# Kernel optimization log

Hardware: AMD Instinct MI355X
Metric: run time of the kernel (lower is better)

The kernel has to match this reference:

```python
import jax, jax.numpy as jnp
import numpy as np

HEADS = 4
DIM_HEAD = 32
SCALE = DIM_HEAD ** -0.5
EPS = 1e-5


def setup_inputs() -> dict:
    key = jax.random.key(0)
    ks = jax.random.split(key, 4)
    x = jax.random.normal(ks[0], (8, 64, 32, 32, 32), dtype=jnp.float32)
    w_qkv = jax.random.normal(ks[1], (384, 64), dtype=jnp.float32) * 0.05
    w_out = jax.random.normal(ks[2], (64, 128), dtype=jnp.float32) * 0.05
    b_out = jax.random.normal(ks[3], (64,), dtype=jnp.float32) * 0.05
    gamma = jnp.ones((64,), dtype=jnp.float32)
    beta = jnp.zeros((64,), dtype=jnp.float32)
    return {"x": x, "w_qkv": w_qkv, "w_out": w_out, "b_out": b_out,
            "gamma": gamma, "beta": beta}


def reference(x, w_qkv, w_out, b_out, gamma, beta):
    b, c, l, h, w = x.shape
    n = l * h * w
    xf = x.reshape(b, c, n)
    # 1x1 Conv3d (no bias) == channel matmul
    qkv = jnp.einsum('oc,bcn->bon', w_qkv, xf)            # [b, 3*H*D, n]
    q, k, v = jnp.split(qkv, 3, axis=1)
    def to_heads(t):
        return t.reshape(b, HEADS, DIM_HEAD, n)            # [b, H, D, n]
    q, k, v = to_heads(q), to_heads(k), to_heads(v)
    q = jax.nn.softmax(q, axis=2) * SCALE                  # softmax over head dim
    k = jax.nn.softmax(k, axis=3)                          # softmax over tokens
    context = jnp.einsum('bhdn,bhen->bhde', k, v)          # [b, H, D, D]
    out = jnp.einsum('bhde,bhdn->bhen', context, q)        # [b, H, D, n]
    out = out.reshape(b, HEADS * DIM_HEAD, n)
    # to_out: 1x1 Conv3d with bias, then GroupNorm(1, dim)
    out = jnp.einsum('oc,bcn->bon', w_out, out) + b_out[None, :, None]
    mu = out.mean(axis=(1, 2), keepdims=True)
    var = out.var(axis=(1, 2), keepdims=True)
    out = (out - mu) * jax.lax.rsqrt(var + EPS)
    out = out * gamma[None, :, None] + beta[None, :, None]
    return out.reshape(b, c, l, h, w)
```

## Files before the change

### kernel.cpp

```cpp
#include <hip/hip_runtime.h>

typedef unsigned short u16;
typedef __bf16 bf16;
typedef __bf16 bf16x8 __attribute__((ext_vector_type(8)));
typedef float f32x4 __attribute__((ext_vector_type(4)));

#define NTOK 32768
#define SCALE_F 0.17677669529663689f

__device__ __forceinline__ u16 f2bf(float f){
  unsigned u = __builtin_bit_cast(unsigned, f);
  u += 0x7fffu + ((u>>16)&1u);
  return (u16)(u>>16);
}
__device__ __forceinline__ float bf2f(u16 u){
  unsigned v = ((unsigned)u)<<16;
  return __builtin_bit_cast(float, v);
}

__global__ __launch_bounds__(256) void k1_ctx(const float* __restrict__ x,
    const float* __restrict__ wqkv, float* __restrict__ ctxP, float* __restrict__ s1P)
{
  const int b = blockIdx.y, chunk = blockIdx.x;
  const int t = threadIdx.x, w = t>>6, l = t&63, lr = l&15, lg = l>>4;
  __shared__ u16 xT[64*72];
  __shared__ u16 ek[128*72];
  __shared__ u16 vl[128*72];

  bf16x8 afr[4][2];
  #pragma unroll
  for (int rt=0;rt<4;rt++)
    #pragma unroll
    for (int ks=0;ks<2;ks++){
      const float* src = wqkv + (128 + w*64 + rt*16 + lr)*64 + ks*32 + lg*8;
      #pragma unroll
      for (int j=0;j<8;j++) ((u16*)&afr[rt][ks])[j] = f2bf(src[j]);
    }

  f32x4 ctx[2][2];
  #pragma unroll
  for (int i=0;i<2;i++)
    #pragma unroll
    for (int j=0;j<2;j++) ctx[i][j] = f32x4{0.f,0.f,0.f,0.f};
  float s1a = 0.f;
  const float* xb = x + (long)b*64*NTOK;

  for (int s=0; s<8; s++) {
    const int n0 = chunk*512 + s*64;
    __syncthreads();
    {
      const int c = t>>2, j0 = (t&3)*16;
      #pragma unroll
      for (int i=0;i<4;i++){
        f32x4 v4 = *(const f32x4*)(xb + (long)c*NTOK + n0 + j0 + i*4);
        #pragma unroll
        for (int j=0;j<4;j++) xT[(j0+i*4+j)*72 + c] = f2bf(v4[j]);
      }
    }
    __syncthreads();
    f32x4 acc[4][4];
    #pragma unroll
    for (int rt=0;rt<4;rt++)
      #pragma unroll
      for (int ct=0;ct<4;ct++) acc[rt][ct] = f32x4{0.f,0.f,0.f,0.f};
    #pragma unroll
    for (int ks=0;ks<2;ks++){
      bf16x8 bfr[4];
      #pragma unroll
      for (int ct=0;ct<4;ct++)
        bfr[ct] = *(const bf16x8*)&xT[(ct*16+lr)*72 + ks*32 + lg*8];
      #pragma unroll
      for (int rt=0;rt<4;rt++){
        #pragma unroll
        for (int ct=0;ct<4;ct++)
          acc[rt][ct] = __builtin_amdgcn_mfma_f32_16x16x32_bf16(afr[rt][ks], bfr[ct], acc[rt][ct], 0,0,0);
      }
    }
    if (w < 2) {
      #pragma unroll
      for (int rt=0;rt<4;rt++)
        #pragma unroll
        for (int ct=0;ct<4;ct++)
          #pragma unroll
          for (int ri=0;ri<4;ri++){
            const int ch = w*64 + rt*16 + lg*4 + ri;
            ek[ch*72 + ct*16 + lr] = f2bf(__expf(acc[rt][ct][ri]));
          }
    } else {
      #pragma unroll
      for (int rt=0;rt<4;rt++)
        #pragma unroll
        for (int ct=0;ct<4;ct++)
          #pragma unroll
          for (int ri=0;ri<4;ri++){
            const int ch = (w-2)*64 + rt*16 + lg*4 + ri;
            vl[ch*72 + ct*16 + lr] = f2bf(acc[rt][ct][ri]);
          }
    }
    __syncthreads();
    #pragma unroll
    for (int ks=0;ks<2;ks++){
      bf16x8 bd[2];
      #pragma unroll
      for (int cd=0;cd<2;cd++)
        bd[cd] = *(const bf16x8*)&ek[(w*32 + cd*16 + lr)*72 + ks*32 + lg*8];
      #pragma unroll
      for (int re=0;re<2;re++){
        bf16x8 a = *(const bf16x8*)&vl[(w*32 + re*16 + lr)*72 + ks*32 + lg*8];
        #pragma unroll
        for (int cd=0;cd<2;cd++)
          ctx[re][cd] = __builtin_amdgcn_mfma_f32_16x16x32_bf16(a, bd[cd], ctx[re][cd], 0,0,0);
      }
    }
    {
      const int ch = t>>1, c0 = (t&1)*32;
      float sacc = 0.f;
      #pragma unroll
      for (int j=0;j<32;j++) sacc += bf2f(ek[ch*72 + c0 + j]);
      s1a += sacc;
    }
  }
  float* cp = ctxP + (((long)b*64 + chunk)*4 + w)*1024;
  #pragma unroll
  for (int re=0;re<2;re++)
    #pragma unroll
    for (int cd=0;cd<2;cd++)
      #pragma unroll
      for (int ri=0;ri<4;ri++){
        const int e = re*16 + lg*4 + ri, d = cd*16 + lr;
        cp[e*32 + d] = ctx[re][cd][ri];
      }
  const float o = __shfl_xor(s1a, 1, 64);
  if ((t&1)==0) s1P[((long)b*64 + chunk)*128 + (t>>1)] = s1a + o;
}

__global__ __launch_bounds__(256) void k2_w2(const float* __restrict__ ctxP,
    const float* __restrict__ s1P, const float* __restrict__ wout, u16* __restrict__ W2)
{
  const int b = blockIdx.y, h = blockIdx.x, t = threadIdx.x;
  __shared__ float cs[1024];
  __shared__ float s1s[32];
  const float* base = ctxP + ((long)b*256 + h)*1024 + t*4;
  float a0=0.f,a1=0.f,a2=0.f,a3=0.f;
  for (int ch=0; ch<64; ch++){
    f32x4 p4 = *(const f32x4*)(base + (long)ch*4096);
    a0 += p4[0]; a1 += p4[1]; a2 += p4[2]; a3 += p4[3];
  }
  cs[t*4+0]=a0; cs[t*4+1]=a1; cs[t*4+2]=a2; cs[t*4+3]=a3;
  if (t < 32){
    float s = 0.f;
    for (int ch=0; ch<64; ch++) s += s1P[((long)b*64+ch)*128 + h*32 + t];
    s1s[t] = s;
  }
  __syncthreads();
  const int d = t & 31;
  const float rinv = SCALE_F / s1s[d];
  #pragma unroll
  for (int oi=0; oi<8; oi++){
    const int o = (t>>5)*8 + oi;
    float acc = 0.f;
    #pragma unroll
    for (int e=0;e<32;e++) acc += wout[o*128 + h*32 + e] * cs[e*32 + d];
    W2[((long)b*64 + o)*128 + h*32 + d] = f2bf(acc * rinv);
  }
}

__global__ __launch_bounds__(256) void k3_y(const float* __restrict__ x,
    const float* __restrict__ wqkv, const u16* __restrict__ W2,
    const float* __restrict__ bout, float* __restrict__ y, float* __restrict__ ysum)
{
  const int b = blockIdx.y, blk = blockIdx.x;
  const int t = threadIdx.x, w = t>>6, l = t&63, lr = l&15, lg = l>>4;
  const int n0 = blk*64;
  __shared__ u16 xT[64*72];
  __shared__ u16 qs[64*136];
  __shared__ float red[8];
  const float* xb = x + (long)b*64*NTOK;

  bf16x8 qfr[2][2];
  #pragma unroll
  for (int rt=0;rt<2;rt++)
    #pragma unroll
    for (int ks=0;ks<2;ks++){
      const float* src = wqkv + (w*32 + rt*16 + lr)*64 + ks*32 + lg*8;
      #pragma unroll
      for (int j=0;j<8;j++) ((u16*)&qfr[rt][ks])[j] = f2bf(src[j]);
    }

  {
    const int c = t>>2, j0 = (t&3)*16;
    #pragma unroll
    for (int i=0;i<4;i++){
      f32x4 v4 = *(const f32x4*)(xb + (long)c*NTOK + n0 + j0 + i*4);
      #pragma unroll
      for (int j=0;j<4;j++) xT[(j0+i*4+j)*72 + c] = f2bf(v4[j]);
    }
  }
  __syncthreads();
  f32x4 qa[2][4];
  #pragma unroll
  for (int rt=0;rt<2;rt++)
    #pragma unroll
    for (int ct=0;ct<4;ct++) qa[rt][ct] = f32x4{0.f,0.f,0.f,0.f};
  #pragma unroll
  for (int ks=0;ks<2;ks++){
    bf16x8 bfr[4];
    #pragma unroll
    for (int ct=0;ct<4;ct++)
      bfr[ct] = *(const bf16x8*)&xT[(ct*16+lr)*72 + ks*32 + lg*8];
    #pragma unroll
    for (int rt=0;rt<2;rt++){
      #pragma unroll
      for (int ct=0;ct<4;ct++)
        qa[rt][ct] = __builtin_amdgcn_mfma_f32_16x16x32_bf16(qfr[rt][ks], bfr[ct], qa[rt][ct], 0,0,0);
    }
  }
  #pragma unroll
  for (int ct=0;ct<4;ct++){
    float e[2][4]; float p = 0.f;
    #pragma unroll
    for (int rt=0;rt<2;rt++)
      #pragma unroll
      for (int ri=0;ri<4;ri++){ e[rt][ri] = __expf(qa[rt][ct][ri]); p += e[rt][ri]; }
    p += __shfl_xor(p, 16, 64);
    p += __shfl_xor(p, 32, 64);
    const float rinv = 1.f/p;
    const int nn = ct*16 + lr;
    #pragma unroll
    for (int rt=0;rt<2;rt++)
      #pragma unroll
      for (int ri=0;ri<4;ri++)
        qs[nn*136 + w*32 + rt*16 + lg*4 + ri] = f2bf(e[rt][ri]*rinv);
  }
  __syncthreads();
  f32x4 ya[4];
  #pragma unroll
  for (int rt=0;rt<4;rt++) ya[rt] = f32x4{0.f,0.f,0.f,0.f};
  #pragma unroll
  for (int ks=0;ks<4;ks++){
    bf16x8 bq = *(const bf16x8*)&qs[(w*16+lr)*136 + ks*32 + lg*8];
    #pragma unroll
    for (int rt=0;rt<4;rt++){
      bf16x8 a = *(const bf16x8*)(W2 + (long)b*8192 + (rt*16+lr)*128 + ks*32 + lg*8);
      ya[rt] = __builtin_amdgcn_mfma_f32_16x16x32_bf16(a, bq, ya[rt], 0,0,0);
    }
  }
  float sum=0.f, ss=0.f;
  float* yb = y + (long)b*64*NTOK;
  #pragma unroll
  for (int rt=0;rt<4;rt++)
    #pragma unroll
    for (int ri=0;ri<4;ri++){
      const int o = rt*16 + lg*4 + ri;
      const int nn = n0 + w*16 + lr;
      const float val = ya[rt][ri] + bout[o];
      sum += val; ss += val*val;
      yb[(long)o*NTOK + nn] = val;
    }
  #pragma unroll
  for (int off=1; off<64; off<<=1){
    sum += __shfl_xor(sum, off, 64);
    ss  += __shfl_xor(ss,  off, 64);
  }
  if (l==0){ red[w*2] = sum; red[w*2+1] = ss; }
  __syncthreads();
  if (t==0){
    ysum[((long)b*512 + blk)*2]   = red[0]+red[2]+red[4]+red[6];
    ysum[((long)b*512 + blk)*2+1] = red[1]+red[3]+red[5]+red[7];
  }
}

__global__ __launch_bounds__(256) void k3b_stats(const float* __restrict__ ysum,
                                                 float* __restrict__ musig)
{
  const int b = blockIdx.x, t = threadIdx.x, w = t>>6, l = t&63;
  float s=0.f, q=0.f;
  for (int i=t; i<512; i+=256){
    s += ysum[((long)b*512+i)*2];
    q += ysum[((long)b*512+i)*2+1];
  }
  #pragma unroll
  for (int off=1; off<64; off<<=1){ s += __shfl_xor(s,off,64); q += __shfl_xor(q,off,64); }
  __shared__ float rs[4], rq[4];
  if (l==0){ rs[w]=s; rq[w]=q; }
  __syncthreads();
  if (t==0){
    const float S = rs[0]+rs[1]+rs[2]+rs[3];
    const float Q = rq[0]+rq[1]+rq[2]+rq[3];
    const float inv_n = 1.f/2097152.f;
    const float mu = S*inv_n;
    const float var = Q*inv_n - mu*mu;
    musig[b*2]   = mu;
    musig[b*2+1] = rsqrtf(var + 1e-5f);
  }
}

__global__ __launch_bounds__(256) void k4_norm(float* __restrict__ y,
    const float* __restrict__ musig, const float* __restrict__ gamma,
    const float* __restrict__ beta)
{
  const long idx = ((long)blockIdx.x*256 + threadIdx.x)*4;
  const int b = (int)(idx >> 21);
  const int c = (int)((idx >> 15) & 63);
  const float mu = musig[b*2], inv = musig[b*2+1];
  const float g = gamma[c]*inv, be = beta[c];
  f32x4 v4 = *(const f32x4*)(y + idx);
  #pragma unroll
  for (int j=0;j<4;j++) v4[j] = (v4[j] - mu)*g + be;
  *(f32x4*)(y + idx) = v4;
}

extern "C" void kernel_launch(void* const* d_in, const int* in_sizes, int n_in,
                              void* d_out, int out_size, void* d_ws, size_t ws_size,
                              hipStream_t stream) {
  const float* x     = (const float*)d_in[0];
  const float* wqkv  = (const float*)d_in[1];
  const float* wout  = (const float*)d_in[2];
  const float* bout  = (const float*)d_in[3];
  const float* gamma = (const float*)d_in[4];
  const float* beta  = (const float*)d_in[5];
  float* out = (float*)d_out;
  char* ws = (char*)d_ws;
  if (ws_size < 8814656u) return;
  float* ctxP = (float*)(ws + 0);
  float* s1P  = (float*)(ws + 8388608);
  u16*  W2    = (u16*) (ws + 8650752);
  float* ysum = (float*)(ws + 8781824);
  float* musig= (float*)(ws + 8814592);

  k1_ctx   <<<dim3(64,8), 256, 0, stream>>>(x, wqkv, ctxP, s1P);
  k2_w2    <<<dim3(4,8),  256, 0, stream>>>(ctxP, s1P, wout, W2);
  k3_y     <<<dim3(512,8),256, 0, stream>>>(x, wqkv, W2, bout, out, ysum);
  k3b_stats<<<8,          256, 0, stream>>>(ysum, musig);
  k4_norm  <<<16384,      256, 0, stream>>>(out, musig, gamma, beta);
}
```

Before: 121.4 us.

## Double k1 grid, swap MFMA operand roles, vectorize LDS stores, compute key sums via MFMA

The context kernel now launches 128 chunks per batch with half the iterations each when the workspace allows, giving more blocks to fill the GPU. The k/v projection swaps operand roles so accumulator outputs land as contiguous 4-element rows, letting the exp and bf16 results go to LDS as vectorized stores instead of scattered scalar writes. The per-channel sum of exp(k) is computed with an extra MFMA against a ones vector instead of a scalar LDS reduction loop. The x tile load is changed to per-token gathers with 16-byte LDS stores, and the same change is made in k3_y. Risks are extra partials for k2 to reduce and strided, less coalesced global reads of x.

```diff
diff --git a/kernel.cpp b/kernel.cpp
--- a/kernel.cpp
+++ b/kernel.cpp
@@ -1,9 +1,10 @@
 #include <hip/hip_runtime.h>
 
 typedef unsigned short u16;
-typedef __bf16 bf16;
 typedef __bf16 bf16x8 __attribute__((ext_vector_type(8)));
 typedef float f32x4 __attribute__((ext_vector_type(4)));
+typedef short s16x4 __attribute__((ext_vector_type(4)));
+typedef short s16x8 __attribute__((ext_vector_type(8)));
 
 #define NTOK 32768
 #define SCALE_F 0.17677669529663689f
@@ -13,49 +14,52 @@
   u += 0x7fffu + ((u>>16)&1u);
   return (u16)(u>>16);
 }
-__device__ __forceinline__ float bf2f(u16 u){
-  unsigned v = ((unsigned)u)<<16;
-  return __builtin_bit_cast(float, v);
-}
 
 __global__ __launch_bounds__(256) void k1_ctx(const float* __restrict__ x,
-    const float* __restrict__ wqkv, float* __restrict__ ctxP, float* __restrict__ s1P)
-{
-  const int b = blockIdx.y, chunk = blockIdx.x;
+    const float* __restrict__ wqkv, float* __restrict__ ctxP, float* __restrict__ s1P,
+    int siters)
+{
+  const int b = blockIdx.y, chunk = blockIdx.x, nchunk = gridDim.x;
   const int t = threadIdx.x, w = t>>6, l = t&63, lr = l&15, lg = l>>4;
   __shared__ u16 xT[64*72];
   __shared__ u16 ek[128*72];
   __shared__ u16 vl[128*72];
 
-  bf16x8 afr[4][2];
-  #pragma unroll
-  for (int rt=0;rt<4;rt++)
+  bf16x8 bw[4][2];
+  #pragma unroll
+  for (int ct=0;ct<4;ct++)
     #pragma unroll
     for (int ks=0;ks<2;ks++){
-      const float* src = wqkv + (128 + w*64 + rt*16 + lr)*64 + ks*32 + lg*8;
-      #pragma unroll
-      for (int j=0;j<8;j++) ((u16*)&afr[rt][ks])[j] = f2bf(src[j]);
-    }
-
-  f32x4 ctx[2][2];
-  #pragma unroll
-  for (int i=0;i<2;i++)
+      const float* src = wqkv + (128 + w*64 + ct*16 + lr)*64 + ks*32 + lg*8;
+      #pragma unroll
+      for (int j=0;j<8;j++) ((u16*)&bw[ct][ks])[j] = f2bf(src[j]);
+    }
+  bf16x8 ones;
+  #pragma unroll
+  for (int j=0;j<8;j++) ((u16*)&ones)[j] = 0x3F80;
+
+  f32x4 ctx[2][2]; f32x4 s1a[2];
+  #pragma unroll
+  for (int i=0;i<2;i++){
+    s1a[i] = f32x4{0.f,0.f,0.f,0.f};
     #pragma unroll
     for (int j=0;j<2;j++) ctx[i][j] = f32x4{0.f,0.f,0.f,0.f};
-  float s1a = 0.f;
+  }
   const float* xb = x + (long)b*64*NTOK;
-
-  for (int s=0; s<8; s++) {
-    const int n0 = chunk*512 + s*64;
+  u16* dst = (w<2) ? ek : vl;
+  const int chb = (w&1)*64;
+  const bool isk = (w<2);
+  const int sn = t&63, cg = (t>>6)*16;
+
+  for (int s=0; s<siters; s++) {
+    const int n0 = (chunk*siters + s)*64;
     __syncthreads();
     {
-      const int c = t>>2, j0 = (t&3)*16;
-      #pragma unroll
-      for (int i=0;i<4;i++){
-        f32x4 v4 = *(const f32x4*)(xb + (long)c*NTOK + n0 + j0 + i*4);
-        #pragma unroll
-        for (int j=0;j<4;j++) xT[(j0+i*4+j)*72 + c] = f2bf(v4[j]);
-      }
+      u16 tmp[16];
+      #pragma unroll
+      for (int i=0;i<16;i++) tmp[i] = f2bf(xb[(long)(cg+i)*NTOK + n0 + sn]);
+      *(s16x8*)&xT[sn*72 + cg]     = *(s16x8*)&tmp[0];
+      *(s16x8*)&xT[sn*72 + cg + 8] = *(s16x8*)&tmp[8];
     }
     __syncthreads();
     f32x4 acc[4][4];
@@ -65,37 +69,29 @@
       for (int ct=0;ct<4;ct++) acc[rt][ct] = f32x4{0.f,0.f,0.f,0.f};
     #pragma unroll
     for (int ks=0;ks<2;ks++){
-      bf16x8 bfr[4];
-      #pragma unroll
-      for (int ct=0;ct<4;ct++)
-        bfr[ct] = *(const bf16x8*)&xT[(ct*16+lr)*72 + ks*32 + lg*8];
-      #pragma unroll
-      for (int rt=0;rt<4;rt++){
-        #pragma unroll
-        for (int ct=0;ct<4;ct++)
-          acc[rt][ct] = __builtin_amdgcn_mfma_f32_16x16x32_bf16(afr[rt][ks], bfr[ct], acc[rt][ct], 0,0,0);
-      }
-    }
-    if (w < 2) {
+      bf16x8 af[4];
+      #pragma unroll
+      for (int rt=0;rt<4;rt++)
+        af[rt] = *(const bf16x8*)&xT[(rt*16+lr)*72 + ks*32 + lg*8];
       #pragma unroll
       for (int rt=0;rt<4;rt++)
         #pragma unroll
         for (int ct=0;ct<4;ct++)
-          #pragma unroll
-          for (int ri=0;ri<4;ri++){
-            const int ch = w*64 + rt*16 + lg*4 + ri;
-            ek[ch*72 + ct*16 + lr] = f2bf(__expf(acc[rt][ct][ri]));
-          }
-    } else {
-      #pragma unroll
-      for (int rt=0;rt<4;rt++)
+          acc[rt][ct] = __builtin_amdgcn_mfma_f32_16x16x32_bf16(af[rt], bw[ct][ks], acc[rt][ct], 0,0,0);
+    }
+    #pragma unroll
+    for (int ct=0;ct<4;ct++){
+      const int row = chb + ct*16 + lr;
+      #pragma unroll
+      for (int rt=0;rt<4;rt++){
+        s16x4 p;
         #pragma unroll
-        for (int ct=0;ct<4;ct++)
-          #pragma unroll
-          for (int ri=0;ri<4;ri++){
-            const int ch = (w-2)*64 + rt*16 + lg*4 + ri;
-            vl[ch*72 + ct*16 + lr] = f2bf(acc[rt][ct][ri]);
-          }
+        for (int ri=0;ri<4;ri++){
+          const float v = acc[rt][ct][ri];
+          p[ri] = (short)f2bf(isk ? __expf(v) : v);
+        }
+        *(s16x4*)&dst[row*72 + rt*16 + lg*4] = p;
+      }
     }
     __syncthreads();
     #pragma unroll
@@ -111,16 +107,12 @@
         for (int cd=0;cd<2;cd++)
           ctx[re][cd] = __builtin_amdgcn_mfma_f32_16x16x32_bf16(a, bd[cd], ctx[re][cd], 0,0,0);
       }
-    }
-    {
-      const int ch = t>>1, c0 = (t&1)*32;
-      float sacc = 0.f;
-      #pragma unroll
-      for (int j=0;j<32;j++) sacc += bf2f(ek[ch*72 + c0 + j]);
-      s1a += sacc;
-    }
-  }
-  float* cp = ctxP + (((long)b*64 + chunk)*4 + w)*1024;
+      #pragma unroll
+      for (int cd=0;cd<2;cd++)
+        s1a[cd] = __builtin_amdgcn_mfma_f32_16x16x32_bf16(ones, bd[cd], s1a[cd], 0,0,0);
+    }
+  }
+  float* cp = ctxP + (((long)b*nchunk + chunk)*4 + w)*1024;
   #pragma unroll
   for (int re=0;re<2;re++)
     #pragma unroll
@@ -130,26 +122,30 @@
         const int e = re*16 + lg*4 + ri, d = cd*16 + lr;
         cp[e*32 + d] = ctx[re][cd][ri];
       }
-  const float o = __shfl_xor(s1a, 1, 64);
-  if ((t&1)==0) s1P[((long)b*64 + chunk)*128 + (t>>1)] = s1a + o;
+  if (lg==0){
+    #pragma unroll
+    for (int cd=0;cd<2;cd++)
+      s1P[((long)b*nchunk + chunk)*128 + w*32 + cd*16 + lr] = s1a[cd][0];
+  }
 }
 
 __global__ __launch_bounds__(256) void k2_w2(const float* __restrict__ ctxP,
-    const float* __restrict__ s1P, const float* __restrict__ wout, u16* __restrict__ W2)
+    const float* __restrict__ s1P, const float* __restrict__ wout, u16* __restrict__ W2,
+    int nchunk)
 {
   const int b = blockIdx.y, h = blockIdx.x, t = threadIdx.x;
   __shared__ float cs[1024];
   __shared__ float s1s[32];
-  const float* base = ctxP + ((long)b*256 + h)*1024 + t*4;
+  const float* base = ctxP + (long)b*nchunk*4096 + h*1024 + t*4;
   float a0=0.f,a1=0.f,a2=0.f,a3=0.f;
-  for (int ch=0; ch<64; ch++){
+  for (int ch=0; ch<nchunk; ch++){
     f32x4 p4 = *(const f32x4*)(base + (long)ch*4096);
     a0 += p4[0]; a1 += p4[1]; a2 += p4[2]; a3 += p4[3];
   }
   cs[t*4+0]=a0; cs[t*4+1]=a1; cs[t*4+2]=a2; cs[t*4+3]=a3;
   if (t < 32){
     float s = 0.f;
-    for (int ch=0; ch<64; ch++) s += s1P[((long)b*64+ch)*128 + h*32 + t];
+    for (int ch=0; ch<nchunk; ch++) s += s1P[((long)b*nchunk+ch)*128 + h*32 + t];
     s1s[t] = s;
   }
   __syncthreads();
@@ -188,13 +184,12 @@
     }
 
   {
-    const int c = t>>2, j0 = (t&3)*16;
-    #pragma unroll
-    for (int i=0;i<4;i++){
-      f32x4 v4 = *(const f32x4*)(xb + (long)c*NTOK + n0 + j0 + i*4);
-      #pragma unroll
-      for (int j=0;j<4;j++) xT[(j0+i*4+j)*72 + c] = f2bf(v4[j]);
-    }
+    const int sn = t&63, cg = (t>>6)*16;
+    u16 tmp[16];
+    #pragma unroll
+    for (int i=0;i<16;i++) tmp[i] = f2bf(xb[(long)(cg+i)*NTOK + n0 + sn]);
+    *(s16x8*)&xT[sn*72 + cg]     = *(s16x8*)&tmp[0];
+    *(s16x8*)&xT[sn*72 + cg + 8] = *(s16x8*)&tmp[8];
   }
   __syncthreads();
   f32x4 qa[2][4];
@@ -227,10 +222,12 @@
     const float rinv = 1.f/p;
     const int nn = ct*16 + lr;
     #pragma unroll
-    for (int rt=0;rt<2;rt++)
-      #pragma unroll
-      for (int ri=0;ri<4;ri++)
-        qs[nn*136 + w*32 + rt*16 + lg*4 + ri] = f2bf(e[rt][ri]*rinv);
+    for (int rt=0;rt<2;rt++){
+      s16x4 pk;
+      #pragma unroll
+      for (int ri=0;ri<4;ri++) pk[ri] = (short)f2bf(e[rt][ri]*rinv);
+      *(s16x4*)&qs[nn*136 + w*32 + rt*16 + lg*4] = pk;
+    }
   }
   __syncthreads();
   f32x4 ya[4];
@@ -321,15 +318,22 @@
   const float* beta  = (const float*)d_in[5];
   float* out = (float*)d_out;
   char* ws = (char*)d_ws;
-  if (ws_size < 8814656u) return;
-  float* ctxP = (float*)(ws + 0);
-  float* s1P  = (float*)(ws + 8388608);
-  u16*  W2    = (u16*) (ws + 8650752);
-  float* ysum = (float*)(ws + 8781824);
-  float* musig= (float*)(ws + 8814592);
-
-  k1_ctx   <<<dim3(64,8), 256, 0, stream>>>(x, wqkv, ctxP, s1P);
-  k2_w2    <<<dim3(4,8),  256, 0, stream>>>(ctxP, s1P, wout, W2);
+
+  int nchunk, siters;
+  size_t need128 = (size_t)131072*128 + (size_t)4096*128 + 131072 + 32768 + 64;
+  if (ws_size >= need128) { nchunk = 128; siters = 4; }
+  else if (ws_size >= (size_t)131072*64 + (size_t)4096*64 + 131072 + 32768 + 64) { nchunk = 64; siters = 8; }
+  else return;
+
+  size_t off = 0;
+  float* ctxP = (float*)(ws + off); off += (size_t)131072*nchunk;
+  float* s1P  = (float*)(ws + off); off += (size_t)4096*nchunk;
+  u16*  W2    = (u16*) (ws + off); off += 131072;
+  float* ysum = (float*)(ws + off); off += 32768;
+  float* musig= (float*)(ws + off);
+
+  k1_ctx   <<<dim3(nchunk,8), 256, 0, stream>>>(x, wqkv, ctxP, s1P, siters);
+  k2_w2    <<<dim3(4,8),  256, 0, stream>>>(ctxP, s1P, wout, W2, nchunk);
   k3_y     <<<dim3(512,8),256, 0, stream>>>(x, wqkv, W2, bout, out, ysum);
   k3b_stats<<<8,          256, 0, stream>>>(ysum, musig);
   k4_norm  <<<16384,      256, 0, stream>>>(out, musig, gamma, beta);
```

Measured after the change: 190.9 us. 1.57x slower.
